# Performance work log

Hardware: AMD Instinct MI355X
Metric: run time of the kernel (lower is better)

Reference implementation:

```python
import jax, jax.numpy as jnp
import numpy as np

LR = 0.1
N_HEADS = 4


def setup_inputs() -> dict:
    key = jax.random.key(0)
    ks = jax.random.split(key, 12)
    B, S, D, M, H = 2, 1024, 128, 512, 512
    s = 0.05
    return {
        "x": jax.random.normal(ks[0], (B, S, D), jnp.float32),
        "memory": jax.random.normal(ks[1], (M, D), jnp.float32) * s,
        "w_q": jax.random.normal(ks[2], (D, D), jnp.float32) * s,
        "w_k": jax.random.normal(ks[3], (D, D), jnp.float32) * s,
        "w_v": jax.random.normal(ks[4], (D, D), jnp.float32) * s,
        "b_q": jax.random.normal(ks[5], (D,), jnp.float32) * s,
        "b_k": jax.random.normal(ks[6], (D,), jnp.float32) * s,
        "b_v": jax.random.normal(ks[7], (D,), jnp.float32) * s,
        "w_o": jax.random.normal(ks[8], (D, D), jnp.float32) * s,
        "b_o": jax.random.normal(ks[9], (D,), jnp.float32) * s,
        "w_fc": jax.random.normal(ks[10], (H, D), jnp.float32) * s,
        "b_fc": jax.random.normal(ks[11], (H,), jnp.float32) * s,
    }


def reference(x, memory, w_q, w_k, w_v, b_q, b_k, b_v, w_o, b_o, w_fc, b_fc):
    B, S, D = x.shape
    M = memory.shape[0]
    hd = D // N_HEADS

    # --- LongTermMemory update (broadcast pairwise diff [B,S,M,D]) ---
    diff = x[:, :, None, :] - memory[None, None, :, :]          # [B,S,M,D]
    surprise = jnp.sqrt(jnp.sum(diff * diff, axis=-1, keepdims=True))  # [B,S,M,1]
    agg = jnp.mean(LR * surprise * diff, axis=(0, 1))           # [M,D]
    # torch does memory.data += agg (detached in-place update)
    mem = memory + jax.lax.stop_gradient(agg)                    # [M,D]

    # --- MultiheadAttention(query=x, key=mem, value=mem), batch_first ---
    # mem is identical across batch, so project once.
    q = (x @ w_q.T + b_q).reshape(B, S, N_HEADS, hd)
    k = (mem @ w_k.T + b_k).reshape(M, N_HEADS, hd)
    v = (mem @ w_v.T + b_v).reshape(M, N_HEADS, hd)
    scores = jnp.einsum('bshd,mhd->bhsm', q, k) / jnp.sqrt(jnp.asarray(hd, x.dtype))
    attn = jax.nn.softmax(scores, axis=-1)
    ctx = jnp.einsum('bhsm,mhd->bshd', attn, v).reshape(B, S, D)
    attn_out = ctx @ w_o.T + b_o                                 # [B,S,D]

    # --- Linear + ReLU ---
    return jax.nn.relu(attn_out @ w_fc.T + b_fc)                 # [B,S,hidden]
```

## Files before the change

### kernel.cpp

```cpp
#include <hip/hip_runtime.h>
#include <hip/hip_bf16.h>
#include <math.h>

#define SS 1024
#define MM 512
#define LRC (0.1f/2048.0f)
#define SCALE 0.17677669529663687f

typedef __attribute__((ext_vector_type(8))) short s8v;
typedef __attribute__((ext_vector_type(4))) float f32x4;
#define MFMA16(a, b, c) __builtin_amdgcn_mfma_f32_16x16x32_bf16(a, b, c, 0, 0, 0)

__device__ __forceinline__ unsigned short f2b(float f) {
  union { float f; unsigned int u; } v; v.f = f;
  return (unsigned short)((v.u + 0x7FFFu + ((v.u >> 16) & 1u)) >> 16);
}

__global__ __launch_bounds__(256) void k_p1(
    const float* __restrict__ x, const float* __restrict__ mem,
    const float* __restrict__ wq, const float* __restrict__ wk,
    const float* __restrict__ wv, const float* __restrict__ wo,
    const float* __restrict__ wfc, const float* __restrict__ bq,
    unsigned short* __restrict__ STb, unsigned short* __restrict__ xT,
    unsigned short* __restrict__ qbf,
    unsigned short* __restrict__ wkb, unsigned short* __restrict__ wvb,
    unsigned short* __restrict__ wob, unsigned short* __restrict__ wfcb) {
  __shared__ alignas(16) char smem[69376];
  const int t = threadIdx.x, bx = blockIdx.x;
  const int w = t >> 6, l = t & 63;
  const int kq = (l >> 4) * 8;
  const int r0l = (l >> 4) * 4;

  if (bx < 256) {
    float (*xl)[132]          = reinterpret_cast<float (*)[132]>(smem);
    unsigned short (*xb)[136] = reinterpret_cast<unsigned short (*)[136]>(smem + 33792);
    unsigned short (*mb)[136] = reinterpret_cast<unsigned short (*)[136]>(smem + 51200);
    float* xn                 = reinterpret_cast<float*>(smem + 68608);
    float* mn                 = reinterpret_cast<float*>(smem + 68864);
    const int bs0 = (bx & 31) * 64, m0 = (bx >> 5) * 64;

    for (int i = t; i < 2048; i += 256) {
      int r = i >> 5, c4 = (i & 31) * 4;
      float4 v = *reinterpret_cast<const float4*>(&x[(bs0 + r) * 128 + c4]);
      xl[r][c4] = v.x; xl[r][c4+1] = v.y; xl[r][c4+2] = v.z; xl[r][c4+3] = v.w;
      ushort4 u; u.x = f2b(v.x); u.y = f2b(v.y); u.z = f2b(v.z); u.w = f2b(v.w);
      *reinterpret_cast<ushort4*>(&xb[r][c4]) = u;
    }
    __syncthreads();
    {
      int r = t >> 2, q = t & 3;
      float s = 0.f;
      #pragma unroll
      for (int j = 0; j < 32; ++j) { float v = xl[r][q * 32 + j]; s += v * v; }
      s += __shfl_xor(s, 1); s += __shfl_xor(s, 2);
      if (q == 0) xn[r] = s;
    }
    if ((bx >> 5) == 0) {
      int d = t >> 1, hh = t & 1;
      #pragma unroll
      for (int j4 = 0; j4 < 32; j4 += 4) {
        ushort4 u;
        u.x = xb[hh*32 + j4    ][d];
        u.y = xb[hh*32 + j4 + 1][d];
        u.z = xb[hh*32 + j4 + 2][d];
        u.w = xb[hh*32 + j4 + 3][d];
        *reinterpret_cast<ushort4*>(&xT[d * 2048 + bs0 + hh*32 + j4]) = u;
      }
    }
    __syncthreads();
    for (int i = t; i < 2048; i += 256) {
      int r = i >> 5, c4 = (i & 31) * 4;
      float4 v = *reinterpret_cast<const float4*>(&mem[(m0 + r) * 128 + c4]);
      xl[r][c4] = v.x; xl[r][c4+1] = v.y; xl[r][c4+2] = v.z; xl[r][c4+3] = v.w;
      ushort4 u; u.x = f2b(v.x); u.y = f2b(v.y); u.z = f2b(v.z); u.w = f2b(v.w);
      *reinterpret_cast<ushort4*>(&mb[r][c4]) = u;
    }
    __syncthreads();
    {
      int r = t >> 2, q = t & 3;
      float s = 0.f;
      #pragma unroll
      for (int j = 0; j < 32; ++j) { float v = xl[r][q * 32 + j]; s += v * v; }
      s += __shfl_xor(s, 1); s += __shfl_xor(s, 2);
      if (q == 0) mn[r] = s;
    }
    __syncthreads();
    f32x4 acc[4] = {};
    #pragma unroll
    for (int kc = 0; kc < 4; ++kc) {
      s8v a = *reinterpret_cast<const s8v*>(&xb[w*16 + (l&15)][kc*32 + kq]);
      #pragma unroll
      for (int mt = 0; mt < 4; ++mt) {
        s8v b = *reinterpret_cast<const s8v*>(&mb[mt*16 + (l&15)][kc*32 + kq]);
        acc[mt] = MFMA16(a, b, acc[mt]);
      }
    }
    const int r0g = bs0 + w * 16 + r0l;
    float xnr[4];
    #pragma unroll
    for (int i = 0; i < 4; ++i) xnr[i] = xn[w*16 + r0l + i];
    #pragma unroll
    for (int mt = 0; mt < 4; ++mt) {
      const int coll = mt * 16 + (l & 15);
      const float mnv = mn[coll];
      ushort4 u;
      u.x = f2b(sqrtf(fmaxf(0.f, xnr[0] + mnv - 2.f * acc[mt][0])));
      u.y = f2b(sqrtf(fmaxf(0.f, xnr[1] + mnv - 2.f * acc[mt][1])));
      u.z = f2b(sqrtf(fmaxf(0.f, xnr[2] + mnv - 2.f * acc[mt][2])));
      u.w = f2b(sqrtf(fmaxf(0.f, xnr[3] + mnv - 2.f * acc[mt][3])));
      *reinterpret_cast<ushort4*>(&STb[(m0 + coll) * 2048 + r0g]) = u;
    }
  } else if (bx < 288) {
    unsigned short (*xb)[136]  = reinterpret_cast<unsigned short (*)[136]>(smem);
    unsigned short (*wql)[136] = reinterpret_cast<unsigned short (*)[136]>(smem + 17408);
    const int s0 = (bx - 256) * 64;
    for (int i = t; i < 2048; i += 256) {
      int r = i >> 5, c4 = (i & 31) * 4;
      float4 v = *reinterpret_cast<const float4*>(&x[(s0 + r) * 128 + c4]);
      ushort4 u; u.x = f2b(v.x); u.y = f2b(v.y); u.z = f2b(v.z); u.w = f2b(v.w);
      *reinterpret_cast<ushort4*>(&xb[r][c4]) = u;
    }
    for (int i = t; i < 4096; i += 256) {
      int r = i >> 5, c4 = (i & 31) * 4;
      float4 v = *reinterpret_cast<const float4*>(&wq[r * 128 + c4]);
      ushort4 u; u.x = f2b(v.x); u.y = f2b(v.y); u.z = f2b(v.z); u.w = f2b(v.w);
      *reinterpret_cast<ushort4*>(&wql[r][c4]) = u;
    }
    __syncthreads();
    f32x4 acc[8] = {};
    #pragma unroll
    for (int kc = 0; kc < 4; ++kc) {
      s8v a = *reinterpret_cast<const s8v*>(&xb[w*16 + (l&15)][kc*32 + kq]);
      #pragma unroll
      for (int nt = 0; nt < 8; ++nt) {
        s8v b = *reinterpret_cast<const s8v*>(&wql[nt*16 + (l&15)][kc*32 + kq]);
        acc[nt] = MFMA16(a, b, acc[nt]);
      }
    }
    const int r0g = s0 + w * 16 + r0l;
    #pragma unroll
    for (int nt = 0; nt < 8; ++nt) {
      const int col = nt * 16 + (l & 15);
      const float bb = bq[col];
      #pragma unroll
      for (int i = 0; i < 4; ++i)
        qbf[(r0g + i) * 128 + col] = f2b((acc[nt][i] + bb) * SCALE);
    }
  } else {
    const float* src; unsigned short* dst; int off = 0;
    if (bx == 288)      { src = wk;  dst = wkb; }
    else if (bx == 289) { src = wv;  dst = wvb; }
    else if (bx == 290) { src = wo;  dst = wob; }
    else                { src = wfc; dst = wfcb; off = (bx - 291) * 16384; }
    for (int i = t; i < 4096; i += 256) {
      float4 v = *reinterpret_cast<const float4*>(&src[off + i * 4]);
      ushort4 u; u.x = f2b(v.x); u.y = f2b(v.y); u.z = f2b(v.z); u.w = f2b(v.w);
      *reinterpret_cast<ushort4*>(&dst[off + i * 4]) = u;
    }
  }
}

__global__ __launch_bounds__(256) void k_p2(
    const unsigned short* __restrict__ STb, const unsigned short* __restrict__ xT,
    const float* __restrict__ mem,
    const unsigned short* __restrict__ wkb, const unsigned short* __restrict__ wvb,
    const float* __restrict__ bk, const float* __restrict__ bv,
    unsigned short* __restrict__ kbf, unsigned short* __restrict__ vT) {
  __shared__ float Tld[16][132];
  __shared__ float srowl[16];
  __shared__ unsigned short mnl[16][136];
  const int t = threadIdx.x;
  const int w = t >> 6, l = t & 63;
  const int kq = (l >> 4) * 8;
  const int r0l = (l >> 4) * 4;
  const int m0 = blockIdx.x * 16;

  f32x4 acc[2] = {};
  float ssum = 0.f;
  const int arow = m0 + (l & 15);
  #pragma unroll 4
  for (int kk = 0; kk < 64; ++kk) {
    s8v a = *reinterpret_cast<const s8v*>(&STb[arow * 2048 + kk * 32 + kq]);
    #pragma unroll
    for (int j = 0; j < 8; ++j) {
      union { unsigned int u; float f; } cv;
      cv.u = ((unsigned int)(unsigned short)a[j]) << 16;
      ssum += cv.f;
    }
    #pragma unroll
    for (int nt = 0; nt < 2; ++nt) {
      s8v b = *reinterpret_cast<const s8v*>(&xT[(w*32 + nt*16 + (l&15)) * 2048 + kk*32 + kq]);
      acc[nt] = MFMA16(a, b, acc[nt]);
    }
  }
  ssum += __shfl_xor(ssum, 16); ssum += __shfl_xor(ssum, 32);
  if (w == 0 && l < 16) srowl[l] = ssum;
  #pragma unroll
  for (int nt = 0; nt < 2; ++nt) {
    const int col = w * 32 + nt * 16 + (l & 15);
    #pragma unroll
    for (int i = 0; i < 4; ++i) Tld[r0l + i][col] = acc[nt][i];
  }
  __syncthreads();
  #pragma unroll
  for (int i = 0; i < 8; ++i) {
    const int flat = t + 256 * i;
    const int r = flat >> 7, c = flat & 127;
    const float mv = mem[(m0 + r) * 128 + c];
    mnl[r][c] = f2b(mv + LRC * (Tld[r][c] - srowl[r] * mv));
  }
  __syncthreads();
  #pragma unroll
  for (int p = 0; p < 2; ++p) {
    const unsigned short* W = p ? wvb : wkb;
    const float* bias = p ? bv : bk;
    f32x4 pacc[2] = {};
    #pragma unroll
    for (int kc = 0; kc < 4; ++kc) {
      s8v a = *reinterpret_cast<const s8v*>(&mnl[l & 15][kc * 32 + kq]);
      #pragma unroll
      for (int nt = 0; nt < 2; ++nt) {
        s8v b = *reinterpret_cast<const s8v*>(&W[(w*32 + nt*16 + (l&15)) * 128 + kc*32 + kq]);
        pacc[nt] = MFMA16(a, b, pacc[nt]);
      }
    }
    #pragma unroll
    for (int nt = 0; nt < 2; ++nt) {
      const int col = w * 32 + nt * 16 + (l & 15);
      const float bb = bias[col];
      if (p == 0) {
        #pragma unroll
        for (int i = 0; i < 4; ++i)
          kbf[(m0 + r0l + i) * 128 + col] = f2b(pacc[nt][i] + bb);
      } else {
        ushort4 u;
        u.x = f2b(pacc[nt][0] + bb); u.y = f2b(pacc[nt][1] + bb);
        u.z = f2b(pacc[nt][2] + bb); u.w = f2b(pacc[nt][3] + bb);
        *reinterpret_cast<ushort4*>(&vT[col * 512 + m0 + r0l]) = u;
      }
    }
  }
}

__global__ __launch_bounds__(256) void k_p3(
    const unsigned short* __restrict__ qbf, const unsigned short* __restrict__ kbf,
    const unsigned short* __restrict__ vT, const unsigned short* __restrict__ wob,
    const unsigned short* __restrict__ wfcb, const float* __restrict__ bo,
    const float* __restrict__ bfc, float* __restrict__ out) {
  __shared__ alignas(16) char smem[75264];
  unsigned short (*Pl)[520] = reinterpret_cast<unsigned short (*)[520]>(smem);
  unsigned short (*cl)[136] = reinterpret_cast<unsigned short (*)[136]>(smem + 66560);
  unsigned short (*al)[136] = reinterpret_cast<unsigned short (*)[136]>(smem + 70912);
  const int t = threadIdx.x;
  const int w = t >> 6, l = t & 63;
  const int kq = (l >> 4) * 8;
  const int r0l = (l >> 4) * 4;
  const int r0 = blockIdx.x * 16;

  {
    const int h = w;
    const s8v a = *reinterpret_cast<const s8v*>(&qbf[(r0 + (l & 15)) * 128 + h * 32 + kq]);
    f32x4 acc[32];
    #pragma unroll
    for (int mt = 0; mt < 32; ++mt) acc[mt] = f32x4{0.f, 0.f, 0.f, 0.f};
    #pragma unroll
    for (int mt = 0; mt < 32; ++mt) {
      s8v b2 = *reinterpret_cast<const s8v*>(&kbf[(mt*16 + (l&15)) * 128 + h*32 + kq]);
      acc[mt] = MFMA16(a, b2, acc[mt]);
    }
    #pragma unroll
    for (int i = 0; i < 4; ++i) {
      float mx = acc[0][i];
      #pragma unroll
      for (int mt = 1; mt < 32; ++mt) mx = fmaxf(mx, acc[mt][i]);
      mx = fmaxf(mx, __shfl_xor(mx, 1));
      mx = fmaxf(mx, __shfl_xor(mx, 2));
      mx = fmaxf(mx, __shfl_xor(mx, 4));
      mx = fmaxf(mx, __shfl_xor(mx, 8));
      float sm = 0.f;
      #pragma unroll
      for (int mt = 0; mt < 32; ++mt) {
        float e = __expf(acc[mt][i] - mx); acc[mt][i] = e; sm += e;
      }
      sm += __shfl_xor(sm, 1); sm += __shfl_xor(sm, 2);
      sm += __shfl_xor(sm, 4); sm += __shfl_xor(sm, 8);
      const float inv = 1.f / sm;
      #pragma unroll
      for (int mt = 0; mt < 32; ++mt)
        Pl[h * 16 + r0l + i][mt * 16 + (l & 15)] = f2b(acc[mt][i] * inv);
    }
  }
  __syncthreads();
  {
    const int h = w;
    f32x4 acc[2] = {};
    #pragma unroll 4
    for (int kk = 0; kk < 16; ++kk) {
      s8v a = *reinterpret_cast<const s8v*>(&Pl[h * 16 + (l & 15)][kk * 32 + kq]);
      #pragma unroll
      for (int nt = 0; nt < 2; ++nt) {
        s8v b2 = *reinterpret_cast<const s8v*>(&vT[(h*32 + nt*16 + (l&15)) * 512 + kk*32 + kq]);
        acc[nt] = MFMA16(a, b2, acc[nt]);
      }
    }
    #pragma unroll
    for (int nt = 0; nt < 2; ++nt) {
      const int col = h * 32 + nt * 16 + (l & 15);
      #pragma unroll
      for (int i = 0; i < 4; ++i) cl[r0l + i][col] = f2b(acc[nt][i]);
    }
  }
  __syncthreads();
  {
    f32x4 acc[2] = {};
    #pragma unroll
    for (int kc = 0; kc < 4; ++kc) {
      s8v a = *reinterpret_cast<const s8v*>(&cl[l & 15][kc * 32 + kq]);
      #pragma unroll
      for (int nt = 0; nt < 2; ++nt) {
        s8v b2 = *reinterpret_cast<const s8v*>(&wob[(w*32 + nt*16 + (l&15)) * 128 + kc*32 + kq]);
        acc[nt] = MFMA16(a, b2, acc[nt]);
      }
    }
    #pragma unroll
    for (int nt = 0; nt < 2; ++nt) {
      const int col = w * 32 + nt * 16 + (l & 15);
      const float bb = bo[col];
      #pragma unroll
      for (int i = 0; i < 4; ++i) al[r0l + i][col] = f2b(acc[nt][i] + bb);
    }
  }
  __syncthreads();
  {
    f32x4 acc[8] = {};
    #pragma unroll
    for (int kc = 0; kc < 4; ++kc) {
      s8v a = *reinterpret_cast<const s8v*>(&al[l & 15][kc * 32 + kq]);
      #pragma unroll
      for (int nt = 0; nt < 8; ++nt) {
        s8v b2 = *reinterpret_cast<const s8v*>(&wfcb[(w*128 + nt*16 + (l&15)) * 128 + kc*32 + kq]);
        acc[nt] = MFMA16(a, b2, acc[nt]);
      }
    }
    #pragma unroll
    for (int nt = 0; nt < 8; ++nt) {
      const int col = w * 128 + nt * 16 + (l & 15);
      const float bb = bfc[col];
      #pragma unroll
      for (int i = 0; i < 4; ++i)
        out[(r0 + r0l + i) * 512 + col] = fmaxf(acc[nt][i] + bb, 0.f);
    }
  }
}

extern "C" void kernel_launch(void* const* d_in, const int* in_sizes, int n_in,
                              void* d_out, int out_size, void* d_ws, size_t ws_size,
                              hipStream_t stream) {
  const float* x    = (const float*)d_in[0];
  const float* mem  = (const float*)d_in[1];
  const float* w_q  = (const float*)d_in[2];
  const float* w_k  = (const float*)d_in[3];
  const float* w_v  = (const float*)d_in[4];
  const float* b_q  = (const float*)d_in[5];
  const float* b_k  = (const float*)d_in[6];
  const float* b_v  = (const float*)d_in[7];
  const float* w_o  = (const float*)d_in[8];
  const float* b_o  = (const float*)d_in[9];
  const float* w_fc = (const float*)d_in[10];
  const float* b_fc = (const float*)d_in[11];
  float* out = (float*)d_out;

  char* base = (char*)d_ws;
  unsigned short* STb  = (unsigned short*)(base);
  unsigned short* xT   = (unsigned short*)(base + 2097152);
  unsigned short* qbf  = (unsigned short*)(base + 2621440);
  unsigned short* kbf  = (unsigned short*)(base + 3145728);
  unsigned short* vT   = (unsigned short*)(base + 3276800);
  unsigned short* wkb  = (unsigned short*)(base + 3407872);
  unsigned short* wvb  = (unsigned short*)(base + 3440640);
  unsigned short* wob  = (unsigned short*)(base + 3473408);
  unsigned short* wfcb = (unsigned short*)(base + 3506176);

  k_p1<<<295, 256, 0, stream>>>(x, mem, w_q, w_k, w_v, w_o, w_fc, b_q,
                                STb, xT, qbf, wkb, wvb, wob, wfcb);
  k_p2<<<32, 256, 0, stream>>>(STb, xT, mem, wkb, wvb, b_k, b_v, kbf, vT);
  k_p3<<<128, 256, 0, stream>>>(qbf, kbf, vT, wob, wfcb, b_o, b_fc, out);
}
```

Baseline: 58.91 us.

## Fuse three kernels into one persistent kernel with software grid barriers

Merges the three launches into a single 256-block kernel separated by atomic-counter grid barriers, removing two kernel launch gaps. The q-projection and weight conversion work is moved onto blocks of later phases, so it now runs alongside the memory update or the K/V projection instead of adding extra blocks. Risks include a deadlock if not all 256 blocks are co-resident, the spin-wait cost, the extra memset launch, and the larger shared allocation lowering occupancy.

```diff
diff --git a/kernel.cpp b/kernel.cpp
--- a/kernel.cpp
+++ b/kernel.cpp
@@ -6,6 +6,7 @@
 #define MM 512
 #define LRC (0.1f/2048.0f)
 #define SCALE 0.17677669529663687f
+#define NBLK 256
 
 typedef __attribute__((ext_vector_type(8))) short s8v;
 typedef __attribute__((ext_vector_type(4))) float f32x4;
@@ -16,22 +17,48 @@
   return (unsigned short)((v.u + 0x7FFFu + ((v.u >> 16) & 1u)) >> 16);
 }
 
-__global__ __launch_bounds__(256) void k_p1(
+__device__ __forceinline__ void grid_barrier(int* bar) {
+  __syncthreads();
+  if (threadIdx.x == 0) {
+    int* cnt = bar;
+    int* gen = bar + 1;
+    __threadfence();
+    const int g = __hip_atomic_load(gen, __ATOMIC_RELAXED, __HIP_MEMORY_SCOPE_AGENT);
+    const int prev = __hip_atomic_fetch_add(cnt, 1, __ATOMIC_ACQ_REL, __HIP_MEMORY_SCOPE_AGENT);
+    if (prev == NBLK - 1) {
+      __hip_atomic_store(cnt, 0, __ATOMIC_RELAXED, __HIP_MEMORY_SCOPE_AGENT);
+      __hip_atomic_store(gen, g + 1, __ATOMIC_RELEASE, __HIP_MEMORY_SCOPE_AGENT);
+    } else {
+      while (__hip_atomic_load(gen, __ATOMIC_ACQUIRE, __HIP_MEMORY_SCOPE_AGENT) == g) {
+        __builtin_amdgcn_s_sleep(8);
+      }
+    }
+    __threadfence();
+  }
+  __syncthreads();
+}
+
+__global__ __launch_bounds__(256) void k_mega(
     const float* __restrict__ x, const float* __restrict__ mem,
     const float* __restrict__ wq, const float* __restrict__ wk,
     const float* __restrict__ wv, const float* __restrict__ wo,
-    const float* __restrict__ wfc, const float* __restrict__ bq,
+    const float* __restrict__ wfc,
+    const float* __restrict__ bq, const float* __restrict__ bk,
+    const float* __restrict__ bv, const float* __restrict__ bo,
+    const float* __restrict__ bfc,
     unsigned short* __restrict__ STb, unsigned short* __restrict__ xT,
-    unsigned short* __restrict__ qbf,
+    unsigned short* __restrict__ qbf, unsigned short* __restrict__ kbf,
+    unsigned short* __restrict__ vT,
     unsigned short* __restrict__ wkb, unsigned short* __restrict__ wvb,
-    unsigned short* __restrict__ wob, unsigned short* __restrict__ wfcb) {
-  __shared__ alignas(16) char smem[69376];
+    unsigned short* __restrict__ wob, unsigned short* __restrict__ wfcb,
+    int* __restrict__ bar, float* __restrict__ out) {
+  __shared__ alignas(16) char smem[75264];
   const int t = threadIdx.x, bx = blockIdx.x;
   const int w = t >> 6, l = t & 63;
   const int kq = (l >> 4) * 8;
   const int r0l = (l >> 4) * 4;
 
-  if (bx < 256) {
+  {
     float (*xl)[132]          = reinterpret_cast<float (*)[132]>(smem);
     unsigned short (*xb)[136] = reinterpret_cast<unsigned short (*)[136]>(smem + 33792);
     unsigned short (*mb)[136] = reinterpret_cast<unsigned short (*)[136]>(smem + 51200);
@@ -110,10 +137,95 @@
       u.w = f2b(sqrtf(fmaxf(0.f, xnr[3] + mnv - 2.f * acc[mt][3])));
       *reinterpret_cast<ushort4*>(&STb[(m0 + coll) * 2048 + r0g]) = u;
     }
-  } else if (bx < 288) {
+    if (bx >= 249) {
+      const float* src; unsigned short* dst; int off = 0;
+      if (bx == 249)      { src = wk;  dst = wkb; }
+      else if (bx == 250) { src = wv;  dst = wvb; }
+      else if (bx == 251) { src = wo;  dst = wob; }
+      else                { src = wfc; dst = wfcb; off = (bx - 252) * 16384; }
+      for (int i = t; i < 4096; i += 256) {
+        float4 v = *reinterpret_cast<const float4*>(&src[off + i * 4]);
+        ushort4 u; u.x = f2b(v.x); u.y = f2b(v.y); u.z = f2b(v.z); u.w = f2b(v.w);
+        *reinterpret_cast<ushort4*>(&dst[off + i * 4]) = u;
+      }
+    }
+  }
+  grid_barrier(bar);
+
+  if (bx < 32) {
+    float (*Tld)[132] = reinterpret_cast<float (*)[132]>(smem);
+    float* srowl      = reinterpret_cast<float*>(smem + 8448);
+    unsigned short (*mnl)[136] = reinterpret_cast<unsigned short (*)[136]>(smem + 8512);
+    const int m0 = bx * 16;
+    f32x4 acc[2] = {};
+    float ssum = 0.f;
+    const int arow = m0 + (l & 15);
+    #pragma unroll 4
+    for (int kk = 0; kk < 64; ++kk) {
+      s8v a = *reinterpret_cast<const s8v*>(&STb[arow * 2048 + kk * 32 + kq]);
+      #pragma unroll
+      for (int j = 0; j < 8; ++j) {
+        union { unsigned int u; float f; } cv;
+        cv.u = ((unsigned int)(unsigned short)a[j]) << 16;
+        ssum += cv.f;
+      }
+      #pragma unroll
+      for (int nt = 0; nt < 2; ++nt) {
+        s8v b = *reinterpret_cast<const s8v*>(&xT[(w*32 + nt*16 + (l&15)) * 2048 + kk*32 + kq]);
+        acc[nt] = MFMA16(a, b, acc[nt]);
+      }
+    }
+    ssum += __shfl_xor(ssum, 16); ssum += __shfl_xor(ssum, 32);
+    if (w == 0 && l < 16) srowl[l] = ssum;
+    #pragma unroll
+    for (int nt = 0; nt < 2; ++nt) {
+      const int col = w * 32 + nt * 16 + (l & 15);
+      #pragma unroll
+      for (int i = 0; i < 4; ++i) Tld[r0l + i][col] = acc[nt][i];
+    }
+    __syncthreads();
+    #pragma unroll
+    for (int i = 0; i < 8; ++i) {
+      const int flat = t + 256 * i;
+      const int r = flat >> 7, c = flat & 127;
+      const float mv = mem[(m0 + r) * 128 + c];
+      mnl[r][c] = f2b(mv + LRC * (Tld[r][c] - srowl[r] * mv));
+    }
+    __syncthreads();
+    #pragma unroll
+    for (int p = 0; p < 2; ++p) {
+      const unsigned short* W = p ? wvb : wkb;
+      const float* bias = p ? bv : bk;
+      f32x4 pacc[2] = {};
+      #pragma unroll
+      for (int kc = 0; kc < 4; ++kc) {
+        s8v a = *reinterpret_cast<const s8v*>(&mnl[l & 15][kc * 32 + kq]);
+        #pragma unroll
+        for (int nt = 0; nt < 2; ++nt) {
+          s8v b = *reinterpret_cast<const s8v*>(&W[(w*32 + nt*16 + (l&15)) * 128 + kc*32 + kq]);
+          pacc[nt] = MFMA16(a, b, pacc[nt]);
+        }
+      }
+      #pragma unroll
+      for (int nt = 0; nt < 2; ++nt) {
+        const int col = w * 32 + nt * 16 + (l & 15);
+        const float bb = bias[col];
+        if (p == 0) {
+          #pragma unroll
+          for (int i = 0; i < 4; ++i)
+            kbf[(m0 + r0l + i) * 128 + col] = f2b(pacc[nt][i] + bb);
+        } else {
+          ushort4 u;
+          u.x = f2b(pacc[nt][0] + bb); u.y = f2b(pacc[nt][1] + bb);
+          u.z = f2b(pacc[nt][2] + bb); u.w = f2b(pacc[nt][3] + bb);
+          *reinterpret_cast<ushort4*>(&vT[col * 512 + m0 + r0l]) = u;
+        }
+      }
+    }
+  } else if (bx < 64) {
     unsigned short (*xb)[136]  = reinterpret_cast<unsigned short (*)[136]>(smem);
     unsigned short (*wql)[136] = reinterpret_cast<unsigned short (*)[136]>(smem + 17408);
-    const int s0 = (bx - 256) * 64;
+    const int s0 = (bx - 32) * 64;
     for (int i = t; i < 2048; i += 256) {
       int r = i >> 5, c4 = (i & 31) * 4;
       float4 v = *reinterpret_cast<const float4*>(&x[(s0 + r) * 128 + c4]);
@@ -146,209 +258,108 @@
       for (int i = 0; i < 4; ++i)
         qbf[(r0g + i) * 128 + col] = f2b((acc[nt][i] + bb) * SCALE);
     }
-  } else {
-    const float* src; unsigned short* dst; int off = 0;
-    if (bx == 288)      { src = wk;  dst = wkb; }
-    else if (bx == 289) { src = wv;  dst = wvb; }
-    else if (bx == 290) { src = wo;  dst = wob; }
-    else                { src = wfc; dst = wfcb; off = (bx - 291) * 16384; }
-    for (int i = t; i < 4096; i += 256) {
-      float4 v = *reinterpret_cast<const float4*>(&src[off + i * 4]);
-      ushort4 u; u.x = f2b(v.x); u.y = f2b(v.y); u.z = f2b(v.z); u.w = f2b(v.w);
-      *reinterpret_cast<ushort4*>(&dst[off + i * 4]) = u;
-    }
   }
-}
-
-__global__ __launch_bounds__(256) void k_p2(
-    const unsigned short* __restrict__ STb, const unsigned short* __restrict__ xT,
-    const float* __restrict__ mem,
-    const unsigned short* __restrict__ wkb, const unsigned short* __restrict__ wvb,
-    const float* __restrict__ bk, const float* __restrict__ bv,
-    unsigned short* __restrict__ kbf, unsigned short* __restrict__ vT) {
-  __shared__ float Tld[16][132];
-  __shared__ float srowl[16];
-  __shared__ unsigned short mnl[16][136];
-  const int t = threadIdx.x;
-  const int w = t >> 6, l = t & 63;
-  const int kq = (l >> 4) * 8;
-  const int r0l = (l >> 4) * 4;
-  const int m0 = blockIdx.x * 16;
-
-  f32x4 acc[2] = {};
-  float ssum = 0.f;
-  const int arow = m0 + (l & 15);
-  #pragma unroll 4
-  for (int kk = 0; kk < 64; ++kk) {
-    s8v a = *reinterpret_cast<const s8v*>(&STb[arow * 2048 + kk * 32 + kq]);
-    #pragma unroll
-    for (int j = 0; j < 8; ++j) {
-      union { unsigned int u; float f; } cv;
-      cv.u = ((unsigned int)(unsigned short)a[j]) << 16;
-      ssum += cv.f;
-    }
-    #pragma unroll
-    for (int nt = 0; nt < 2; ++nt) {
-      s8v b = *reinterpret_cast<const s8v*>(&xT[(w*32 + nt*16 + (l&15)) * 2048 + kk*32 + kq]);
-      acc[nt] = MFMA16(a, b, acc[nt]);
-    }
-  }
-  ssum += __shfl_xor(ssum, 16); ssum += __shfl_xor(ssum, 32);
-  if (w == 0 && l < 16) srowl[l] = ssum;
-  #pragma unroll
-  for (int nt = 0; nt < 2; ++nt) {
-    const int col = w * 32 + nt * 16 + (l & 15);
-    #pragma unroll
-    for (int i = 0; i < 4; ++i) Tld[r0l + i][col] = acc[nt][i];
-  }
-  __syncthreads();
-  #pragma unroll
-  for (int i = 0; i < 8; ++i) {
-    const int flat = t + 256 * i;
-    const int r = flat >> 7, c = flat & 127;
-    const float mv = mem[(m0 + r) * 128 + c];
-    mnl[r][c] = f2b(mv + LRC * (Tld[r][c] - srowl[r] * mv));
-  }
-  __syncthreads();
-  #pragma unroll
-  for (int p = 0; p < 2; ++p) {
-    const unsigned short* W = p ? wvb : wkb;
-    const float* bias = p ? bv : bk;
-    f32x4 pacc[2] = {};
-    #pragma unroll
-    for (int kc = 0; kc < 4; ++kc) {
-      s8v a = *reinterpret_cast<const s8v*>(&mnl[l & 15][kc * 32 + kq]);
+  grid_barrier(bar);
+
+  if (bx < 128) {
+    unsigned short (*Pl)[520] = reinterpret_cast<unsigned short (*)[520]>(smem);
+    unsigned short (*cl)[136] = reinterpret_cast<unsigned short (*)[136]>(smem + 66560);
+    unsigned short (*al)[136] = reinterpret_cast<unsigned short (*)[136]>(smem + 70912);
+    const int r0 = bx * 16;
+
+    {
+      const int h = w;
+      const s8v a = *reinterpret_cast<const s8v*>(&qbf[(r0 + (l & 15)) * 128 + h * 32 + kq]);
+      f32x4 acc[32];
+      #pragma unroll
+      for (int mt = 0; mt < 32; ++mt) acc[mt] = f32x4{0.f, 0.f, 0.f, 0.f};
+      #pragma unroll
+      for (int mt = 0; mt < 32; ++mt) {
+        s8v b2 = *reinterpret_cast<const s8v*>(&kbf[(mt*16 + (l&15)) * 128 + h*32 + kq]);
+        acc[mt] = MFMA16(a, b2, acc[mt]);
+      }
+      #pragma unroll
+      for (int i = 0; i < 4; ++i) {
+        float mx = acc[0][i];
+        #pragma unroll
+        for (int mt = 1; mt < 32; ++mt) mx = fmaxf(mx, acc[mt][i]);
+        mx = fmaxf(mx, __shfl_xor(mx, 1));
+        mx = fmaxf(mx, __shfl_xor(mx, 2));
+        mx = fmaxf(mx, __shfl_xor(mx, 4));
+        mx = fmaxf(mx, __shfl_xor(mx, 8));
+        float sm = 0.f;
+        #pragma unroll
+        for (int mt = 0; mt < 32; ++mt) {
+          float e = __expf(acc[mt][i] - mx); acc[mt][i] = e; sm += e;
+        }
+        sm += __shfl_xor(sm, 1); sm += __shfl_xor(sm, 2);
+        sm += __shfl_xor(sm, 4); sm += __shfl_xor(sm, 8);
+        const float inv = 1.f / sm;
+        #pragma unroll
+        for (int mt = 0; mt < 32; ++mt)
+          Pl[h * 16 + r0l + i][mt * 16 + (l & 15)] = f2b(acc[mt][i] * inv);
+      }
+    }
+    __syncthreads();
+    {
+      const int h = w;
+      f32x4 acc[2] = {};
+      #pragma unroll 4
+      for (int kk = 0; kk < 16; ++kk) {
+        s8v a = *reinterpret_cast<const s8v*>(&Pl[h * 16 + (l & 15)][kk * 32 + kq]);
+        #pragma unroll
+        for (int nt = 0; nt < 2; ++nt) {
+          s8v b2 = *reinterpret_cast<const s8v*>(&vT[(h*32 + nt*16 + (l&15)) * 512 + kk*32 + kq]);
+          acc[nt] = MFMA16(a, b2, acc[nt]);
+        }
+      }
       #pragma unroll
       for (int nt = 0; nt < 2; ++nt) {
-        s8v b = *reinterpret_cast<const s8v*>(&W[(w*32 + nt*16 + (l&15)) * 128 + kc*32 + kq]);
-        pacc[nt] = MFMA16(a, b, pacc[nt]);
-      }
-    }
-    #pragma unroll
-    for (int nt = 0; nt < 2; ++nt) {
-      const int col = w * 32 + nt * 16 + (l & 15);
-      const float bb = bias[col];
-      if (p == 0) {
+        const int col = h * 32 + nt * 16 + (l & 15);
+        #pragma unroll
+        for (int i = 0; i < 4; ++i) cl[r0l + i][col] = f2b(acc[nt][i]);
+      }
+    }
+    __syncthreads();
+    {
+      f32x4 acc[2] = {};
+      #pragma unroll
+      for (int kc = 0; kc < 4; ++kc) {
+        s8v a = *reinterpret_cast<const s8v*>(&cl[l & 15][kc * 32 + kq]);
+        #pragma unroll
+        for (int nt = 0; nt < 2; ++nt) {
+          s8v b2 = *reinterpret_cast<const s8v*>(&wob[(w*32 + nt*16 + (l&15)) * 128 + kc*32 + kq]);
+          acc[nt] = MFMA16(a, b2, acc[nt]);
+        }
+      }
+      #pragma unroll
+      for (int nt = 0; nt < 2; ++nt) {
+        const int col = w * 32 + nt * 16 + (l & 15);
+        const float bb = bo[col];
+        #pragma unroll
+        for (int i = 0; i < 4; ++i) al[r0l + i][col] = f2b(acc[nt][i] + bb);
+      }
+    }
+    __syncthreads();
+    {
+      f32x4 acc[8] = {};
+      #pragma unroll
+      for (int kc = 0; kc < 4; ++kc) {
+        s8v a = *reinterpret_cast<const s8v*>(&al[l & 15][kc * 32 + kq]);
+        #pragma unroll
+        for (int nt = 0; nt < 8; ++nt) {
+          s8v b2 = *reinterpret_cast<const s8v*>(&wfcb[(w*128 + nt*16 + (l&15)) * 128 + kc*32 + kq]);
+          acc[nt] = MFMA16(a, b2, acc[nt]);
+        }
+      }
+      #pragma unroll
+      for (int nt = 0; nt < 8; ++nt) {
+        const int col = w * 128 + nt * 16 + (l & 15);
+        const float bb = bfc[col];
         #pragma unroll
         for (int i = 0; i < 4; ++i)
-          kbf[(m0 + r0l + i) * 128 + col] = f2b(pacc[nt][i] + bb);
-      } else {
-        ushort4 u;
-        u.x = f2b(pacc[nt][0] + bb); u.y = f2b(pacc[nt][1] + bb);
-        u.z = f2b(pacc[nt][2] + bb); u.w = f2b(pacc[nt][3] + bb);
-        *reinterpret_cast<ushort4*>(&vT[col * 512 + m0 + r0l]) = u;
-      }
-    }
-  }
-}
-
-__global__ __launch_bounds__(256) void k_p3(
-    const unsigned short* __restrict__ qbf, const unsigned short* __restrict__ kbf,
-    const unsigned short* __restrict__ vT, const unsigned short* __restrict__ wob,
-    const unsigned short* __restrict__ wfcb, const float* __restrict__ bo,
-    const float* __restrict__ bfc, float* __restrict__ out) {
-  __shared__ alignas(16) char smem[75264];
-  unsigned short (*Pl)[520] = reinterpret_cast<unsigned short (*)[520]>(smem);
-  unsigned short (*cl)[136] = reinterpret_cast<unsigned short (*)[136]>(smem + 66560);
-  unsigned short (*al)[136] = reinterpret_cast<unsigned short (*)[136]>(smem + 70912);
-  const int t = threadIdx.x;
-  const int w = t >> 6, l = t & 63;
-  const int kq = (l >> 4) * 8;
-  const int r0l = (l >> 4) * 4;
-  const int r0 = blockIdx.x * 16;
-
-  {
-    const int h = w;
-    const s8v a = *reinterpret_cast<const s8v*>(&qbf[(r0 + (l & 15)) * 128 + h * 32 + kq]);
-    f32x4 acc[32];
-    #pragma unroll
-    for (int mt = 0; mt < 32; ++mt) acc[mt] = f32x4{0.f, 0.f, 0.f, 0.f};
-    #pragma unroll
-    for (int mt = 0; mt < 32; ++mt) {
-      s8v b2 = *reinterpret_cast<const s8v*>(&kbf[(mt*16 + (l&15)) * 128 + h*32 + kq]);
-      acc[mt] = MFMA16(a, b2, acc[mt]);
-    }
-    #pragma unroll
-    for (int i = 0; i < 4; ++i) {
-      float mx = acc[0][i];
-      #pragma unroll
-      for (int mt = 1; mt < 32; ++mt) mx = fmaxf(mx, acc[mt][i]);
-      mx = fmaxf(mx, __shfl_xor(mx, 1));
-      mx = fmaxf(mx, __shfl_xor(mx, 2));
-      mx = fmaxf(mx, __shfl_xor(mx, 4));
-      mx = fmaxf(mx, __shfl_xor(mx, 8));
-      float sm = 0.f;
-      #pragma unroll
-      for (int mt = 0; mt < 32; ++mt) {
-        float e = __expf(acc[mt][i] - mx); acc[mt][i] = e; sm += e;
-      }
-      sm += __shfl_xor(sm, 1); sm += __shfl_xor(sm, 2);
-      sm += __shfl_xor(sm, 4); sm += __shfl_xor(sm, 8);
-      const float inv = 1.f / sm;
-      #pragma unroll
-      for (int mt = 0; mt < 32; ++mt)
-        Pl[h * 16 + r0l + i][mt * 16 + (l & 15)] = f2b(acc[mt][i] * inv);
-    }
-  }
-  __syncthreads();
-  {
-    const int h = w;
-    f32x4 acc[2] = {};
-    #pragma unroll 4
-    for (int kk = 0; kk < 16; ++kk) {
-      s8v a = *reinterpret_cast<const s8v*>(&Pl[h * 16 + (l & 15)][kk * 32 + kq]);
-      #pragma unroll
-      for (int nt = 0; nt < 2; ++nt) {
-        s8v b2 = *reinterpret_cast<const s8v*>(&vT[(h*32 + nt*16 + (l&15)) * 512 + kk*32 + kq]);
-        acc[nt] = MFMA16(a, b2, acc[nt]);
-      }
-    }
-    #pragma unroll
-    for (int nt = 0; nt < 2; ++nt) {
-      const int col = h * 32 + nt * 16 + (l & 15);
-      #pragma unroll
-      for (int i = 0; i < 4; ++i) cl[r0l + i][col] = f2b(acc[nt][i]);
-    }
-  }
-  __syncthreads();
-  {
-    f32x4 acc[2] = {};
-    #pragma unroll
-    for (int kc = 0; kc < 4; ++kc) {
-      s8v a = *reinterpret_cast<const s8v*>(&cl[l & 15][kc * 32 + kq]);
-      #pragma unroll
-      for (int nt = 0; nt < 2; ++nt) {
-        s8v b2 = *reinterpret_cast<const s8v*>(&wob[(w*32 + nt*16 + (l&15)) * 128 + kc*32 + kq]);
-        acc[nt] = MFMA16(a, b2, acc[nt]);
-      }
-    }
-    #pragma unroll
-    for (int nt = 0; nt < 2; ++nt) {
-      const int col = w * 32 + nt * 16 + (l & 15);
-      const float bb = bo[col];
-      #pragma unroll
-      for (int i = 0; i < 4; ++i) al[r0l + i][col] = f2b(acc[nt][i] + bb);
-    }
-  }
-  __syncthreads();
-  {
-    f32x4 acc[8] = {};
-    #pragma unroll
-    for (int kc = 0; kc < 4; ++kc) {
-      s8v a = *reinterpret_cast<const s8v*>(&al[l & 15][kc * 32 + kq]);
-      #pragma unroll
-      for (int nt = 0; nt < 8; ++nt) {
-        s8v b2 = *reinterpret_cast<const s8v*>(&wfcb[(w*128 + nt*16 + (l&15)) * 128 + kc*32 + kq]);
-        acc[nt] = MFMA16(a, b2, acc[nt]);
-      }
-    }
-    #pragma unroll
-    for (int nt = 0; nt < 8; ++nt) {
-      const int col = w * 128 + nt * 16 + (l & 15);
-      const float bb = bfc[col];
-      #pragma unroll
-      for (int i = 0; i < 4; ++i)
-        out[(r0 + r0l + i) * 512 + col] = fmaxf(acc[nt][i] + bb, 0.f);
+          out[(r0 + r0l + i) * 512 + col] = fmaxf(acc[nt][i] + bb, 0.f);
+      }
     }
   }
 }
@@ -380,9 +391,11 @@
   unsigned short* wvb  = (unsigned short*)(base + 3440640);
   unsigned short* wob  = (unsigned short*)(base + 3473408);
   unsigned short* wfcb = (unsigned short*)(base + 3506176);
-
-  k_p1<<<295, 256, 0, stream>>>(x, mem, w_q, w_k, w_v, w_o, w_fc, b_q,
-                                STb, xT, qbf, wkb, wvb, wob, wfcb);
-  k_p2<<<32, 256, 0, stream>>>(STb, xT, mem, wkb, wvb, b_k, b_v, kbf, vT);
-  k_p3<<<128, 256, 0, stream>>>(qbf, kbf, vT, wob, wfcb, b_o, b_fc, out);
+  int* bar             = (int*)(base + 3637248);
+
+  hipMemsetAsync(bar, 0, 8, stream);
+  k_mega<<<NBLK, 256, 0, stream>>>(x, mem, w_q, w_k, w_v, w_o, w_fc,
+                                   b_q, b_k, b_v, b_o, b_fc,
+                                   STb, xT, qbf, kbf, vT,
+                                   wkb, wvb, wob, wfcb, bar, out);
 }
```

New measurement: 153.6 us. +160.8%, slower.

## Fuse norm computation into loads and move surprise row-sum into p1

Applied to the files above, without the earlier changes.

The p1 distance blocks now compute squared norms directly from the global float4 loads while converting to bf16. This drops the fp32 staging tile, two barriers and the shared-memory footprint. The per-memory-row sum of surprise values is computed in fp32 in p1's epilogue, written as per-block partials to a workspace buffer, and reduced in p2. This removes the bf16 unpack-and-accumulate from p2's hot MFMA loop, at the cost of an extra shuffle/LDS reduction in p1 and a small extra global buffer.

```diff
diff --git a/kernel.cpp b/kernel.cpp
--- a/kernel.cpp
+++ b/kernel.cpp
@@ -22,39 +22,49 @@
     const float* __restrict__ wv, const float* __restrict__ wo,
     const float* __restrict__ wfc, const float* __restrict__ bq,
     unsigned short* __restrict__ STb, unsigned short* __restrict__ xT,
-    unsigned short* __restrict__ qbf,
+    unsigned short* __restrict__ qbf, float* __restrict__ srowp,
     unsigned short* __restrict__ wkb, unsigned short* __restrict__ wvb,
     unsigned short* __restrict__ wob, unsigned short* __restrict__ wfcb) {
-  __shared__ alignas(16) char smem[69376];
+  __shared__ alignas(16) char smem[52224];
   const int t = threadIdx.x, bx = blockIdx.x;
   const int w = t >> 6, l = t & 63;
   const int kq = (l >> 4) * 8;
   const int r0l = (l >> 4) * 4;
 
   if (bx < 256) {
-    float (*xl)[132]          = reinterpret_cast<float (*)[132]>(smem);
-    unsigned short (*xb)[136] = reinterpret_cast<unsigned short (*)[136]>(smem + 33792);
-    unsigned short (*mb)[136] = reinterpret_cast<unsigned short (*)[136]>(smem + 51200);
-    float* xn                 = reinterpret_cast<float*>(smem + 68608);
-    float* mn                 = reinterpret_cast<float*>(smem + 68864);
+    unsigned short (*xb)[136] = reinterpret_cast<unsigned short (*)[136]>(smem);
+    unsigned short (*mb)[136] = reinterpret_cast<unsigned short (*)[136]>(smem + 17408);
+    float* xn                 = reinterpret_cast<float*>(smem + 34816);
+    float* mn                 = reinterpret_cast<float*>(smem + 35072);
+    float (*red)[64]          = reinterpret_cast<float (*)[64]>(smem + 35328);
     const int bs0 = (bx & 31) * 64, m0 = (bx >> 5) * 64;
 
-    for (int i = t; i < 2048; i += 256) {
-      int r = i >> 5, c4 = (i & 31) * 4;
-      float4 v = *reinterpret_cast<const float4*>(&x[(bs0 + r) * 128 + c4]);
-      xl[r][c4] = v.x; xl[r][c4+1] = v.y; xl[r][c4+2] = v.z; xl[r][c4+3] = v.w;
-      ushort4 u; u.x = f2b(v.x); u.y = f2b(v.y); u.z = f2b(v.z); u.w = f2b(v.w);
-      *reinterpret_cast<ushort4*>(&xb[r][c4]) = u;
-    }
-    __syncthreads();
     {
-      int r = t >> 2, q = t & 3;
+      const int r = t >> 2, q = t & 3;
+      const float* xp = &x[(bs0 + r) * 128 + q * 32];
       float s = 0.f;
       #pragma unroll
-      for (int j = 0; j < 32; ++j) { float v = xl[r][q * 32 + j]; s += v * v; }
+      for (int j4 = 0; j4 < 32; j4 += 4) {
+        float4 v = *reinterpret_cast<const float4*>(xp + j4);
+        s += v.x*v.x + v.y*v.y + v.z*v.z + v.w*v.w;
+        ushort4 u; u.x = f2b(v.x); u.y = f2b(v.y); u.z = f2b(v.z); u.w = f2b(v.w);
+        *reinterpret_cast<ushort4*>(&xb[r][q*32 + j4]) = u;
+      }
       s += __shfl_xor(s, 1); s += __shfl_xor(s, 2);
       if (q == 0) xn[r] = s;
-    }
+      const float* mp = &mem[(m0 + r) * 128 + q * 32];
+      float sm_ = 0.f;
+      #pragma unroll
+      for (int j4 = 0; j4 < 32; j4 += 4) {
+        float4 v = *reinterpret_cast<const float4*>(mp + j4);
+        sm_ += v.x*v.x + v.y*v.y + v.z*v.z + v.w*v.w;
+        ushort4 u; u.x = f2b(v.x); u.y = f2b(v.y); u.z = f2b(v.z); u.w = f2b(v.w);
+        *reinterpret_cast<ushort4*>(&mb[r][q*32 + j4]) = u;
+      }
+      sm_ += __shfl_xor(sm_, 1); sm_ += __shfl_xor(sm_, 2);
+      if (q == 0) mn[r] = sm_;
+    }
+    __syncthreads();
     if ((bx >> 5) == 0) {
       int d = t >> 1, hh = t & 1;
       #pragma unroll
@@ -67,24 +77,6 @@
         *reinterpret_cast<ushort4*>(&xT[d * 2048 + bs0 + hh*32 + j4]) = u;
       }
     }
-    __syncthreads();
-    for (int i = t; i < 2048; i += 256) {
-      int r = i >> 5, c4 = (i & 31) * 4;
-      float4 v = *reinterpret_cast<const float4*>(&mem[(m0 + r) * 128 + c4]);
-      xl[r][c4] = v.x; xl[r][c4+1] = v.y; xl[r][c4+2] = v.z; xl[r][c4+3] = v.w;
-      ushort4 u; u.x = f2b(v.x); u.y = f2b(v.y); u.z = f2b(v.z); u.w = f2b(v.w);
-      *reinterpret_cast<ushort4*>(&mb[r][c4]) = u;
-    }
-    __syncthreads();
-    {
-      int r = t >> 2, q = t & 3;
-      float s = 0.f;
-      #pragma unroll
-      for (int j = 0; j < 32; ++j) { float v = xl[r][q * 32 + j]; s += v * v; }
-      s += __shfl_xor(s, 1); s += __shfl_xor(s, 2);
-      if (q == 0) mn[r] = s;
-    }
-    __syncthreads();
     f32x4 acc[4] = {};
     #pragma unroll
     for (int kc = 0; kc < 4; ++kc) {
@@ -103,13 +95,20 @@
     for (int mt = 0; mt < 4; ++mt) {
       const int coll = mt * 16 + (l & 15);
       const float mnv = mn[coll];
-      ushort4 u;
-      u.x = f2b(sqrtf(fmaxf(0.f, xnr[0] + mnv - 2.f * acc[mt][0])));
-      u.y = f2b(sqrtf(fmaxf(0.f, xnr[1] + mnv - 2.f * acc[mt][1])));
-      u.z = f2b(sqrtf(fmaxf(0.f, xnr[2] + mnv - 2.f * acc[mt][2])));
-      u.w = f2b(sqrtf(fmaxf(0.f, xnr[3] + mnv - 2.f * acc[mt][3])));
+      const float s0 = sqrtf(fmaxf(0.f, xnr[0] + mnv - 2.f * acc[mt][0]));
+      const float s1 = sqrtf(fmaxf(0.f, xnr[1] + mnv - 2.f * acc[mt][1]));
+      const float s2 = sqrtf(fmaxf(0.f, xnr[2] + mnv - 2.f * acc[mt][2]));
+      const float s3 = sqrtf(fmaxf(0.f, xnr[3] + mnv - 2.f * acc[mt][3]));
+      ushort4 u; u.x = f2b(s0); u.y = f2b(s1); u.z = f2b(s2); u.w = f2b(s3);
       *reinterpret_cast<ushort4*>(&STb[(m0 + coll) * 2048 + r0g]) = u;
-    }
+      float cs = s0 + s1 + s2 + s3;
+      cs += __shfl_xor(cs, 16); cs += __shfl_xor(cs, 32);
+      if (l < 16) red[w][mt*16 + l] = cs;
+    }
+    __syncthreads();
+    if (t < 64)
+      srowp[(bx & 31) * 512 + m0 + t] =
+          red[0][t] + red[1][t] + red[2][t] + red[3][t];
   } else if (bx < 288) {
     unsigned short (*xb)[136]  = reinterpret_cast<unsigned short (*)[136]>(smem);
     unsigned short (*wql)[136] = reinterpret_cast<unsigned short (*)[136]>(smem + 17408);
@@ -162,7 +161,7 @@
 
 __global__ __launch_bounds__(256) void k_p2(
     const unsigned short* __restrict__ STb, const unsigned short* __restrict__ xT,
-    const float* __restrict__ mem,
+    const float* __restrict__ mem, const float* __restrict__ srowp,
     const unsigned short* __restrict__ wkb, const unsigned short* __restrict__ wvb,
     const float* __restrict__ bk, const float* __restrict__ bv,
     unsigned short* __restrict__ kbf, unsigned short* __restrict__ vT) {
@@ -175,26 +174,23 @@
   const int r0l = (l >> 4) * 4;
   const int m0 = blockIdx.x * 16;
 
+  if (t < 16) {
+    float s = 0.f;
+    #pragma unroll
+    for (int c = 0; c < 32; ++c) s += srowp[c * 512 + m0 + t];
+    srowl[t] = s;
+  }
   f32x4 acc[2] = {};
-  float ssum = 0.f;
   const int arow = m0 + (l & 15);
   #pragma unroll 4
   for (int kk = 0; kk < 64; ++kk) {
     s8v a = *reinterpret_cast<const s8v*>(&STb[arow * 2048 + kk * 32 + kq]);
     #pragma unroll
-    for (int j = 0; j < 8; ++j) {
-      union { unsigned int u; float f; } cv;
-      cv.u = ((unsigned int)(unsigned short)a[j]) << 16;
-      ssum += cv.f;
-    }
-    #pragma unroll
     for (int nt = 0; nt < 2; ++nt) {
       s8v b = *reinterpret_cast<const s8v*>(&xT[(w*32 + nt*16 + (l&15)) * 2048 + kk*32 + kq]);
       acc[nt] = MFMA16(a, b, acc[nt]);
     }
   }
-  ssum += __shfl_xor(ssum, 16); ssum += __shfl_xor(ssum, 32);
-  if (w == 0 && l < 16) srowl[l] = ssum;
   #pragma unroll
   for (int nt = 0; nt < 2; ++nt) {
     const int col = w * 32 + nt * 16 + (l & 15);
@@ -380,9 +376,10 @@
   unsigned short* wvb  = (unsigned short*)(base + 3440640);
   unsigned short* wob  = (unsigned short*)(base + 3473408);
   unsigned short* wfcb = (unsigned short*)(base + 3506176);
+  float* srowp         = (float*)(base + 3637248);
 
   k_p1<<<295, 256, 0, stream>>>(x, mem, w_q, w_k, w_v, w_o, w_fc, b_q,
-                                STb, xT, qbf, wkb, wvb, wob, wfcb);
-  k_p2<<<32, 256, 0, stream>>>(STb, xT, mem, wkb, wvb, b_k, b_v, kbf, vT);
+                                STb, xT, qbf, srowp, wkb, wvb, wob, wfcb);
+  k_p2<<<32, 256, 0, stream>>>(STb, xT, mem, srowp, wkb, wvb, b_k, b_v, kbf, vT);
   k_p3<<<128, 256, 0, stream>>>(qbf, kbf, vT, wob, wfcb, b_o, b_fc, out);
 }
```

After: 65.03 us. 10.4% more time.
